# Performance work log

Hardware: AMD Instinct MI355X
Metric: run time of the kernel (lower is better)

The kernel has to match this reference:

```python
import jax, jax.numpy as jnp
import numpy as np

DIM, HK, HV, DK, DV, KC = 2048, 16, 32, 128, 128, 4
B, L = 1, 8192
EPS = 1e-6


def setup_inputs() -> dict:
    key = jax.random.key(0)
    ks = jax.random.split(key, 12)
    conv_dim = 2 * HK * DK + HV * DV  # 8192
    inp = {
        "x": jax.random.normal(ks[0], (B, L, DIM), jnp.float32),
        "cu_seqlens": jnp.array([0, 2048, 4096, 6144, 8192], jnp.int64),
        "Wqkv": jax.random.normal(ks[1], (DIM, conv_dim), jnp.float32) * 0.02,
        "Wz": jax.random.normal(ks[2], (DIM, HV * DV), jnp.float32) * 0.02,
        "Wa": jax.random.normal(ks[3], (DIM, HV), jnp.float32) * 0.02,
        "Wb": jax.random.normal(ks[4], (DIM, HV), jnp.float32) * 0.02,
        "conv_w": jax.random.normal(ks[5], (conv_dim, KC), jnp.float32) * 0.2,
        "A_log": jnp.zeros((HV,), jnp.float32),
        "dt_bias": jnp.ones((HV,), jnp.float32),
        "norm_w": jnp.ones((DV,), jnp.float32),
        "Wout": jax.random.normal(ks[6], (HV * DV, DIM), jnp.float32) * 0.02,
    }
    return inp


def _causal_conv_silu(qkv, conv_w, seq_idx):
    # depthwise causal conv1d with per-sequence masking (channels-last)
    Bb, Ll, C = qkv.shape
    xp = jnp.pad(qkv, ((0, 0), (KC - 1, 0), (0, 0)))
    sp = jnp.pad(seq_idx, ((0, 0), (KC - 1, 0)), constant_values=-1)
    out = jnp.zeros_like(qkv)
    for i in range(KC):
        m = (sp[:, i:i + Ll] == seq_idx)[..., None]
        out = out + conv_w[:, i] * jnp.where(m, xp[:, i:i + Ll], 0.0)
    return jax.nn.silu(out)


def _l2norm(x):
    return x * jax.lax.rsqrt(jnp.sum(x * x, axis=-1, keepdims=True) + EPS)


def reference(x, cu_seqlens, Wqkv, Wz, Wa, Wb, conv_w, A_log, dt_bias, norm_w, Wout):
    Bb, Ll, _ = x.shape
    qkv = x @ Wqkv            # [B,L,conv_dim]
    z = x @ Wz                # [B,L,HV*DV]
    a = x @ Wa                # [B,L,HV]
    b = x @ Wb                # [B,L,HV]

    pos = jnp.arange(Ll)
    seq_idx = jnp.searchsorted(cu_seqlens[1:-1], pos, side="right").astype(jnp.int32)
    seq_idx = jnp.broadcast_to(seq_idx[None, :], (Bb, Ll))

    mixed = _causal_conv_silu(qkv, conv_w, seq_idx)
    key_dim, value_dim = HK * DK, HV * DV
    q, k, v = jnp.split(mixed, [key_dim, 2 * key_dim], axis=-1)
    q = q.reshape(Bb, Ll, HK, DK)
    k = k.reshape(Bb, Ll, HK, DK)
    v = v.reshape(Bb, Ll, HV, DV)
    rep = HV // HK
    q = jnp.repeat(q, rep, axis=2)  # [B,L,HV,DK]
    k = jnp.repeat(k, rep, axis=2)

    # gates
    g = -jnp.exp(A_log) * jax.nn.softplus(a + dt_bias)   # [B,L,HV] (log decay)
    beta = jax.nn.sigmoid(b)                              # [B,L,HV]

    # l2-normed q/k, q scaled
    q = _l2norm(q) * (DK ** -0.5)
    k = _l2norm(k)

    # sequence-start flags for state reset
    starts = jnp.zeros((Ll,), bool).at[cu_seqlens[:-1]].set(True)

    def step(S, inp):
        q_t, k_t, v_t, g_t, b_t, s_t = inp
        S = jnp.where(s_t, 0.0, S)
        S = S * jnp.exp(g_t)[..., None, None]                 # decay
        kv = jnp.einsum("bhk,bhkv->bhv", k_t, S)              # S^T k
        delta = (v_t - kv) * b_t[..., None]
        S = S + k_t[..., :, None] * delta[..., None, :]       # rank-1 delta update
        o = jnp.einsum("bhk,bhkv->bhv", q_t, S)
        return S, o

    S0 = jnp.zeros((Bb, HV, DK, DV), q.dtype)
    xs = (jnp.moveaxis(q, 1, 0), jnp.moveaxis(k, 1, 0), jnp.moveaxis(v, 1, 0),
          jnp.moveaxis(g, 1, 0), jnp.moveaxis(beta, 1, 0), starts)
    _, o = jax.lax.scan(step, S0, xs)                          # [L,B,HV,DV]
    o = jnp.moveaxis(o, 0, 1)                                  # [B,L,HV,DV]

    # gated RMSNorm (gate applied before norm, swish)
    zh = z.reshape(Bb, Ll, HV, DV)
    y = o * jax.nn.silu(zh)
    y = y * jax.lax.rsqrt(jnp.mean(y * y, axis=-1, keepdims=True) + EPS) * norm_w

    return y.reshape(Bb, Ll, HV * DV) @ Wout
```

## Files before the change

kernel.cpp:

```cpp
#include <hip/hip_runtime.h>
#include <hip/hip_bf16.h>
#include <stdint.h>
#include <stdio.h>

#define L_SEQ 8192
#define DIM_ 2048
#define HK_ 16
#define HV_ 32
#define DK_ 128
#define DV_ 128
#define CONV_DIM_ 8192
#define EPS_F 1e-6f

typedef __bf16 bf16;
typedef __bf16 bf16x8 __attribute__((ext_vector_type(8)));
typedef __bf16 bf16x4 __attribute__((ext_vector_type(4)));
typedef __bf16 bf16x2 __attribute__((ext_vector_type(2)));
typedef float f32x4 __attribute__((ext_vector_type(4)));

__device__ __forceinline__ void load_lds16(const void* g, void* l) {
  __builtin_amdgcn_global_load_lds((const __attribute__((address_space(1))) uint32_t*)g,
                                   (__attribute__((address_space(3))) uint32_t*)l,
                                   16, 0, 0);
}

__global__ __launch_bounds__(256) void k_convert(const float4* __restrict__ src,
                                                 bf16x4* __restrict__ dst, int n4) {
  int i = blockIdx.x * 256 + threadIdx.x;
  if (i >= n4) return;
  float4 v = src[i];
  bf16x4 o;
  o[0] = (bf16)v.x; o[1] = (bf16)v.y; o[2] = (bf16)v.z; o[3] = (bf16)v.w;
  dst[i] = o;
}

__global__ __launch_bounds__(256) void k_transpose_cvt(const float* __restrict__ W,
                                                       bf16* __restrict__ Wt, int K, int ldW,
                                                       int n_off) {
  __shared__ float tile[32][33];
  int n0 = blockIdx.x * 32, k0 = blockIdx.y * 32;
  int cx = threadIdx.x & 31, ry = threadIdx.x >> 5;
#pragma unroll
  for (int i = 0; i < 4; i++)
    tile[ry + i * 8][cx] = W[(size_t)(k0 + ry + i * 8) * ldW + n_off + n0 + cx];
  __syncthreads();
#pragma unroll
  for (int i = 0; i < 4; i++) {
    int r = ry + i * 8;
    Wt[(size_t)(n0 + r) * K + k0 + cx] = (bf16)tile[cx][r];
  }
}

template <int BF16_OUT>
__global__ __launch_bounds__(256) void k_gemm_bt(const bf16* __restrict__ A,
                                                 const bf16* __restrict__ Bt,
                                                 void* __restrict__ Cout,
                                                 int M, int N, int K) {
  __shared__ __align__(16) bf16 la[4096];
  __shared__ __align__(16) bf16 lb[4096];
  const int tid = threadIdx.x;
  const int lane = tid & 63;
  const int wave = tid >> 6;
  const int wm = wave >> 1, wn = wave & 1;
  const int bm = blockIdx.y << 7, bn = blockIdx.x << 7;

  f32x4 acc[4][4];
#pragma unroll
  for (int i = 0; i < 4; i++)
#pragma unroll
    for (int j = 0; j < 4; j++) acc[i][j] = (f32x4){0.f, 0.f, 0.f, 0.f};

  const bf16* Ag = A + (size_t)(bm + lane) * K + wave * 8;
  const bf16* Bg = Bt + (size_t)(bn + lane) * K + wave * 8;
  bf16* lA = la + wave * 1024;
  bf16* lB = lb + wave * 1024;
  const size_t rowskip = (size_t)64 * K;

  const int chunk = lane >> 4;
  const int rr = lane & 15;
  const bf16* fa = la + chunk * 1024 + (wm * 64 + rr) * 8;
  const bf16* fb = lb + chunk * 1024 + (wn * 64 + rr) * 8;

  for (int k0 = 0; k0 < K; k0 += 32) {
    __syncthreads();
    load_lds16(Ag + k0, lA);
    load_lds16(Ag + k0 + rowskip, lA + 512);
    load_lds16(Bg + k0, lB);
    load_lds16(Bg + k0 + rowskip, lB + 512);
    __syncthreads();
    bf16x8 af[4], bfr[4];
#pragma unroll
    for (int i = 0; i < 4; i++) {
      af[i] = *(const bf16x8*)(fa + i * 16 * 8);
      bfr[i] = *(const bf16x8*)(fb + i * 16 * 8);
    }
#pragma unroll
    for (int mi = 0; mi < 4; mi++)
#pragma unroll
      for (int ni = 0; ni < 4; ni++)
        acc[mi][ni] = __builtin_amdgcn_mfma_f32_16x16x32_bf16(af[mi], bfr[ni], acc[mi][ni], 0, 0, 0);
  }

  const int col = bn + wn * 64 + rr;
  const int row0 = bm + wm * 64 + (lane >> 4) * 4;
#pragma unroll
  for (int mi = 0; mi < 4; mi++)
#pragma unroll
    for (int ni = 0; ni < 4; ni++)
#pragma unroll
      for (int r = 0; r < 4; r++) {
        int rowi = row0 + mi * 16 + r;
        int coli = col + ni * 16;
        if (BF16_OUT)
          ((bf16*)Cout)[(size_t)rowi * N + coli] = (bf16)acc[mi][ni][r];
        else
          ((float*)Cout)[(size_t)rowi * N + coli] = acc[mi][ni][r];
      }
}

__global__ __launch_bounds__(256) void k_gates(const float* __restrict__ x,
                                               const float* __restrict__ Wa,
                                               const float* __restrict__ Wb,
                                               const float* __restrict__ A_log,
                                               const float* __restrict__ dt_bias,
                                               float* __restrict__ gb) {
  int t = blockIdx.x * 4 + (threadIdx.x >> 6);
  int lane = threadIdx.x & 63;
  int h = lane & 31;
  int isB = lane >> 5;
  const float* W = isB ? Wb : Wa;
  const float* xr = x + (size_t)t * DIM_;
  float a0 = 0.f, a1 = 0.f, a2 = 0.f, a3 = 0.f;
  for (int kk = 0; kk < DIM_; kk += 4) {
    float4 xv = *(const float4*)(xr + kk);
    a0 += xv.x * W[(kk + 0) * 32 + h];
    a1 += xv.y * W[(kk + 1) * 32 + h];
    a2 += xv.z * W[(kk + 2) * 32 + h];
    a3 += xv.w * W[(kk + 3) * 32 + h];
  }
  float acc = (a0 + a1) + (a2 + a3);
  if (isB) {
    gb[(size_t)t * 64 + 32 + h] = 1.f / (1.f + expf(-acc));
  } else {
    float ag = acc + dt_bias[h];
    float sp = (ag > 20.f) ? ag : log1pf(expf(ag));
    gb[(size_t)t * 64 + h] = -expf(A_log[h]) * sp;
  }
}

template <int IS_V>
__global__ __launch_bounds__(128) void k_conv(const bf16* __restrict__ src,
                                              const float* __restrict__ conv_w,
                                              const int* __restrict__ cu, int nseq,
                                              bf16* __restrict__ qn, bf16* __restrict__ kn,
                                              bf16* __restrict__ v) {
  __shared__ float red[2];
  int t = blockIdx.x;
  int grp = blockIdx.y;
  int c = grp * 128 + threadIdx.x;
  int start = 0;
  for (int s = 0; s < nseq; s++) {
    int a = cu[s];
    if (a <= t) start = a;
  }
  float4 w = *(const float4*)(conv_w + (size_t)(c + (IS_V ? 4096 : 0)) * 4);
  float accv = 0.f;
#pragma unroll
  for (int i = 0; i < 4; i++) {
    int tp = t - 3 + i;
    if (tp >= start) {
      float wv = (i == 0) ? w.x : (i == 1) ? w.y : (i == 2) ? w.z : w.w;
      accv += wv * (float)src[(size_t)tp * 4096 + c];
    }
  }
  float val = accv / (1.f + __expf(-accv));
  if (IS_V) {
    v[((size_t)t * HV_ + grp) * DV_ + threadIdx.x] = (bf16)val;
  } else {
    float ss = val * val;
#pragma unroll
    for (int off = 1; off < 64; off <<= 1) ss += __shfl_xor(ss, off);
    if ((threadIdx.x & 63) == 0) red[threadIdx.x >> 6] = ss;
    __syncthreads();
    float tot = red[0] + red[1];
    float scale = rsqrtf(tot + EPS_F);
    if (grp < 16) {
      scale *= 0.08838834764831845f;
      qn[((size_t)t * HK_ + grp) * DK_ + threadIdx.x] = (bf16)(val * scale);
    } else {
      kn[((size_t)t * HK_ + (grp - 16)) * DK_ + threadIdx.x] = (bf16)(val * scale);
    }
  }
}


#define SA_LD 68
#define SUF_LD 65

__device__ __forceinline__ bf16x8 frag256(const bf16* base, int tile, int kk, int lane) {
  int row = tile * 16 + (lane & 15);
  int blk = kk * 4 + (lane >> 4);
  int byte = row * 256 + (((blk & 8) | ((blk & 7) ^ (row & 7))) << 4);
  return *(const bf16x8*)((const char*)base + byte);
}
__device__ __forceinline__ bf16x8 frag128(const bf16* base, int tile, int kk, int lane) {
  int row = tile * 16 + (lane & 15);
  int blk = kk * 4 + (lane >> 4);
  int byte = row * 128 + ((blk ^ (row & 7)) << 4);
  return *(const bf16x8*)((const char*)base + byte);
}
__device__ __forceinline__ bf16x8 ld256v(const bf16* base, int row, int blk) {
  int byte = row * 256 + (((blk & 8) | ((blk & 7) ^ (row & 7))) << 4);
  return *(const bf16x8*)((const char*)base + byte);
}
__device__ __forceinline__ void st128e(bf16* base, int row, int col, float v) {
  int byte = row * 128 + ((((col >> 3) ^ (row & 7)) << 4)) + (col & 7) * 2;
  *(bf16*)((char*)base + byte) = (bf16)v;
}
__device__ __forceinline__ float ld128e(const bf16* base, int row, int col) {
  int byte = row * 128 + ((((col >> 3) ^ (row & 7)) << 4)) + (col & 7) * 2;
  return (float)*(const bf16*)((const char*)base + byte);
}
__device__ __forceinline__ void st256e(bf16* base, int row, int col, float v) {
  int blk = col >> 3;
  int byte = row * 256 + (((blk & 8) | ((blk & 7) ^ (row & 7))) << 4) + (col & 7) * 2;
  *(bf16*)((char*)base + byte) = (bf16)v;
}

__global__ __launch_bounds__(256, 1) void k_scan_chunk(const bf16* __restrict__ qn,
                                                       const bf16* __restrict__ kn,
                                                       const bf16* __restrict__ v,
                                                       const float* __restrict__ gb,
                                                       const int* __restrict__ cu,
                                                       bf16* __restrict__ o) {
  __shared__ __align__(16) bf16 sK[64 * 128];
  __shared__ __align__(16) bf16 sQ[64 * 128];
  __shared__ __align__(16) bf16 sKt[128 * 64];
  __shared__ __align__(16) bf16 sSt[64 * 128];
  __shared__ __align__(16) bf16 sV[64 * 64];
  __shared__ __align__(16) bf16 sM[64 * 64];
  __shared__ __align__(16) bf16 sUt[64 * 64];
  __shared__ float sA[64 * SA_LD];
  __shared__ float sUf[64 * SUF_LD];
  __shared__ float sG2[2][64], sB[2][64], sEg[2][64];

  const int h = blockIdx.y;
  const int hk = h >> 1;
  const int seq = blockIdx.z;
  const int dv0 = blockIdx.x * 64;
  const int tid = threadIdx.x;
  const int lane = tid & 63;
  const int wave = tid >> 6;
  const int w16 = wave * 16;
  const int t0 = cu[seq], t1 = cu[seq + 1];
  if (t0 >= t1) return;

  f32x4 St[2][4];
#pragma unroll
  for (int a = 0; a < 2; a++)
#pragma unroll
    for (int c = 0; c < 4; c++) St[a][c] = (f32x4){0.f, 0.f, 0.f, 0.f};
#pragma unroll
  for (int i = 0; i < 4; i++) ((float4*)sSt)[tid * 4 + i] = (float4){0.f, 0.f, 0.f, 0.f};

  auto stageKQV = [&](int ts) {
#pragma unroll
    for (int it = 0; it < 4; it++) {
      int Bx = (wave * 4 + it) * 64 + lane;
      int r = Bx >> 4, bq = Bx & 15;
      int tr = ts + r; if (tr >= t1) tr = t1 - 1;
      int bs = (bq & 8) | ((bq & 7) ^ (r & 7));
      size_t go = (size_t)tr * (HK_ * DK_) + hk * DK_ + bs * 8;
      load_lds16(kn + go, (char*)sK + (size_t)(wave * 4 + it) * 1024);
      load_lds16(qn + go, (char*)sQ + (size_t)(wave * 4 + it) * 1024);
    }
#pragma unroll
    for (int it = 0; it < 2; it++) {
      int Bx = (wave * 2 + it) * 64 + lane;
      int r = Bx >> 3, bq = Bx & 7;
      int tr = ts + r; if (tr >= t1) tr = t1 - 1;
      int bs = bq ^ (r & 7);
      load_lds16(v + (size_t)tr * (HV_ * DV_) + h * DV_ + dv0 + bs * 8,
                 (char*)sV + (size_t)(wave * 2 + it) * 1024);
    }
  };

  auto prefix = [&](int ts, int pb) {
    int tr = ts + lane;
    float gv = 0.f, bv = 0.f;
    if (tr < t1) {
      gv = gb[(size_t)tr * 64 + h] * 1.44269504088896f;
      bv = gb[(size_t)tr * 64 + 32 + h];
    }
    float ps = gv;
#pragma unroll
    for (int off = 1; off < 64; off <<= 1) {
      float tmp = __shfl_up(ps, off);
      if (lane >= off) ps += tmp;
    }
    sG2[pb][lane] = ps;
    sB[pb][lane] = bv;
    sEg[pb][lane] = exp2f(ps);
  };

  int buf = 0;
  stageKQV(t0);
  if (wave == 0) prefix(t0, 0);
  __syncthreads();

  bool first = true;
  for (int ts = t0; ts < t1; ts += 64) {
    const bool haveNext = (ts + 64 < t1);
    const float* G2 = sG2[buf];
    const float* Bt = sB[buf];
    const float* Eg = sEg[buf];

    f32x4 aKK[4], aQK[4], aKS[4], aQS[4];
#pragma unroll
    for (int c = 0; c < 4; c++) {
      aKK[c] = (f32x4){0.f, 0.f, 0.f, 0.f};
      aQK[c] = (f32x4){0.f, 0.f, 0.f, 0.f};
      aKS[c] = (f32x4){0.f, 0.f, 0.f, 0.f};
      aQS[c] = (f32x4){0.f, 0.f, 0.f, 0.f};
    }
#pragma unroll
    for (int kk = 0; kk < 4; kk++) {
      bf16x8 ak = frag256(sK, wave, kk, lane);
      bf16x8 aq = frag256(sQ, wave, kk, lane);
#pragma unroll
      for (int c = 0; c < 4; c++) {
        if (c <= wave) {
          bf16x8 bk = frag256(sK, c, kk, lane);
          aKK[c] = __builtin_amdgcn_mfma_f32_16x16x32_bf16(ak, bk, aKK[c], 0, 0, 0);
          aQK[c] = __builtin_amdgcn_mfma_f32_16x16x32_bf16(aq, bk, aQK[c], 0, 0, 0);
        }
        if (!first) {
          bf16x8 bs = frag256(sSt, c, kk, lane);
          aKS[c] = __builtin_amdgcn_mfma_f32_16x16x32_bf16(ak, bs, aKS[c], 0, 0, 0);
          aQS[c] = __builtin_amdgcn_mfma_f32_16x16x32_bf16(aq, bs, aQS[c], 0, 0, 0);
        }
      }
    }

    const float G2c = G2[63];
    {
      const int li = lane & 15, lh = lane >> 4;
      float g2s[4];
#pragma unroll
      for (int c = 0; c < 4; c++) g2s[c] = G2[c * 16 + li];
#pragma unroll
      for (int r = 0; r < 4; r++) {
        const int t = w16 + lh * 4 + r;
        const float g2t = G2[t], btv = Bt[t], egt = Eg[t];
#pragma unroll
        for (int c = 0; c < 4; c++) {
          const int s = c * 16 + li;
          const float e = exp2f(g2t - g2s[c]);
          sA[t * SA_LD + s] = (s < t) ? btv * e * aKK[c][r] : 0.f;
          st128e(sM, t, s, (s <= t) ? e * aQK[c][r] : 0.f);
          sUf[t * SUF_LD + s] = btv * (ld128e(sV, t, s) - egt * aKS[c][r]);
        }
      }
    }
    {
      const int t = lane;
      const float sc = exp2f(G2c - G2[t]);
#pragma unroll
      for (int i = 0; i < 4; i++) {
        int dk0 = wave * 32 + i * 8;
        bf16x8 kv = ld256v(sK, t, wave * 4 + i);
#pragma unroll
        for (int j = 0; j < 8; j++) st128e(sKt, dk0 + j, t, (float)kv[j] * sc);
      }
    }
    __syncthreads();

    if (haveNext) {
      stageKQV(ts + 64);
      if (wave == 3) prefix(ts + 64, buf ^ 1);
    }

    for (int b = 0; b < 4; b++) {
      if (wave == 0) {
        const int b16o = b * 16;
        float u[16];
#pragma unroll
        for (int i = 0; i < 16; i++) {
          const int t = b16o + i;
          float x = sUf[t * SUF_LD + lane];
          const float* Ar = &sA[t * SA_LD + b16o];
#pragma unroll
          for (int j = 0; j < i; j++) x -= Ar[j] * u[j];
          u[i] = x;
          sUf[t * SUF_LD + lane] = x;
        }
      }
      __syncthreads();
      if (b < 3) {
        if (wave < 3) {
          const int b16o = b * 16;
          float us[16];
#pragma unroll
          for (int j = 0; j < 16; j++) us[j] = sUf[(b16o + j) * SUF_LD + lane];
          for (int t = b16o + 16 + wave; t < 64; t += 3) {
            float x = sUf[t * SUF_LD + lane];
            const float* Ar = &sA[t * SA_LD + b16o];
#pragma unroll
            for (int j = 0; j < 16; j++) x -= Ar[j] * us[j];
            sUf[t * SUF_LD + lane] = x;
          }
        }
        __syncthreads();
      }
    }

    {
      const int s = lane;
#pragma unroll
      for (int i = 0; i < 16; i++) {
        int dvv = wave * 16 + i;
        st128e(sUt, dvv, s, sUf[s * SUF_LD + dvv]);
      }
    }
    __syncthreads();

    f32x4 aO[4];
#pragma unroll
    for (int c = 0; c < 4; c++)
#pragma unroll
      for (int r = 0; r < 4; r++)
        aO[c][r] = Eg[w16 + (lane >> 4) * 4 + r] * aQS[c][r];
#pragma unroll
    for (int kk = 0; kk < 2; kk++) {
      bf16x8 am = frag128(sM, wave, kk, lane);
#pragma unroll
      for (int c = 0; c < 4; c++) {
        bf16x8 bu = frag128(sUt, c, kk, lane);
        aO[c] = __builtin_amdgcn_mfma_f32_16x16x32_bf16(am, bu, aO[c], 0, 0, 0);
      }
    }
#pragma unroll
    for (int r = 0; r < 4; r++) {
      const int t = w16 + (lane >> 4) * 4 + r;
      if (ts + t < t1) {
#pragma unroll
        for (int c = 0; c < 4; c++)
          o[((size_t)(ts + t) * HV_ + h) * DV_ + dv0 + c * 16 + (lane & 15)] = (bf16)aO[c][r];
      }
    }

    {
      const float egc = Eg[63];
#pragma unroll
      for (int a = 0; a < 2; a++)
#pragma unroll
        for (int c = 0; c < 4; c++)
#pragma unroll
          for (int r = 0; r < 4; r++) St[a][c][r] *= egc;
#pragma unroll
      for (int kk = 0; kk < 2; kk++) {
#pragma unroll
        for (int a = 0; a < 2; a++) {
          bf16x8 akt = frag128(sKt, 2 * wave + a, kk, lane);
#pragma unroll
          for (int c = 0; c < 4; c++) {
            bf16x8 bu = frag128(sUt, c, kk, lane);
            St[a][c] = __builtin_amdgcn_mfma_f32_16x16x32_bf16(akt, bu, St[a][c], 0, 0, 0);
          }
        }
      }
#pragma unroll
      for (int a = 0; a < 2; a++)
#pragma unroll
        for (int c = 0; c < 4; c++)
#pragma unroll
          for (int r = 0; r < 4; r++) {
            int dk = (2 * wave + a) * 16 + (lane >> 4) * 4 + r;
            int dvv = c * 16 + (lane & 15);
            st256e(sSt, dvv, dk, St[a][c][r]);
          }
    }
    first = false;
    buf ^= 1;
    __syncthreads();
  }
}

__global__ __launch_bounds__(256) void k_gatenorm(const bf16* __restrict__ o,
                                                  const bf16* __restrict__ z,
                                                  const float* __restrict__ norm_w,
                                                  bf16* __restrict__ y) {
  int row = blockIdx.x * 4 + (threadIdx.x >> 6);
  int lane = threadIdx.x & 63;
  int i0 = lane * 2;
  bf16x2 ov = *(const bf16x2*)(o + (size_t)row * 128 + i0);
  bf16x2 zv = *(const bf16x2*)(z + (size_t)row * 128 + i0);
  float zf0 = (float)zv[0], zf1 = (float)zv[1];
  float y0 = (float)ov[0] * (zf0 / (1.f + __expf(-zf0)));
  float y1 = (float)ov[1] * (zf1 / (1.f + __expf(-zf1)));
  float ss = y0 * y0 + y1 * y1;
#pragma unroll
  for (int off = 1; off < 64; off <<= 1) ss += __shfl_xor(ss, off);
  float scale = rsqrtf(ss * (1.f / 128.f) + EPS_F);
  float2 nw = *(const float2*)(norm_w + i0);
  bf16x2 out;
  out[0] = (bf16)(y0 * scale * nw.x);
  out[1] = (bf16)(y1 * scale * nw.y);
  *(bf16x2*)(y + (size_t)row * 128 + i0) = out;
}

extern "C" void kernel_launch(void* const* d_in, const int* in_sizes, int n_in,
                              void* d_out, int out_size, void* d_ws, size_t ws_size,
                              hipStream_t stream) {
  const float* x = (const float*)d_in[0];
  const int* cu = (const int*)d_in[1];
  const float* Wqkv = (const float*)d_in[2];
  const float* Wz = (const float*)d_in[3];
  const float* Wa = (const float*)d_in[4];
  const float* Wb = (const float*)d_in[5];
  const float* conv_w = (const float*)d_in[6];
  const float* A_log = (const float*)d_in[7];
  const float* dt_bias = (const float*)d_in[8];
  const float* norm_w = (const float*)d_in[9];
  const float* Wout = (const float*)d_in[10];
  float* out = (float*)d_out;
  const int nseq = in_sizes[1] - 1;

  const size_t MB = 1024 * 1024;
  char* ws = (char*)d_ws;
  bf16* x16   = (bf16*)(ws + 0);
  bf16* WtS   = (bf16*)(ws + 32 * MB);
  bf16* qn    = (bf16*)(ws + 48 * MB);
  bf16* kn    = (bf16*)(ws + 80 * MB);
  bf16* bigA  = (bf16*)(ws + 112 * MB);
  bf16* vbuf  = (bf16*)(ws + 176 * MB);
  float* gb   = (float*)(ws + 240 * MB);
  bf16* z16   = qn;
  bf16* o16   = bigA;
  bf16* y16   = z16;

  if (242 * MB > ws_size) {
    fprintf(stderr, "WORKSPACE TOO SMALL: need %zu, have %zu\n", 242 * MB, ws_size);
    return;
  }

  k_convert<<<(L_SEQ * DIM_ / 4 + 255) / 256, 256, 0, stream>>>((const float4*)x, (bf16x4*)x16,
                                                                L_SEQ * DIM_ / 4);
  k_gates<<<L_SEQ / 4, 256, 0, stream>>>(x, Wa, Wb, A_log, dt_bias, gb);

  k_transpose_cvt<<<dim3(4096 / 32, DIM_ / 32), 256, 0, stream>>>(Wqkv, WtS, DIM_, CONV_DIM_, 0);
  k_gemm_bt<1><<<dim3(4096 / 128, L_SEQ / 128), 256, 0, stream>>>(x16, WtS, bigA, L_SEQ, 4096, DIM_);
  k_conv<0><<<dim3(L_SEQ, 32), 128, 0, stream>>>(bigA, conv_w, cu, nseq, qn, kn, vbuf);

  k_transpose_cvt<<<dim3(4096 / 32, DIM_ / 32), 256, 0, stream>>>(Wqkv, WtS, DIM_, CONV_DIM_, 4096);
  k_gemm_bt<1><<<dim3(4096 / 128, L_SEQ / 128), 256, 0, stream>>>(x16, WtS, bigA, L_SEQ, 4096, DIM_);
  k_conv<1><<<dim3(L_SEQ, 32), 128, 0, stream>>>(bigA, conv_w, cu, nseq, qn, kn, vbuf);

  k_scan_chunk<<<dim3(2, HV_, nseq), 256, 0, stream>>>(qn, kn, vbuf, gb, cu, o16);

  k_transpose_cvt<<<dim3(4096 / 32, DIM_ / 32), 256, 0, stream>>>(Wz, WtS, DIM_, 4096, 0);
  k_gemm_bt<1><<<dim3(4096 / 128, L_SEQ / 128), 256, 0, stream>>>(x16, WtS, z16, L_SEQ, 4096, DIM_);

  k_gatenorm<<<L_SEQ * HV_ / 4, 256, 0, stream>>>(o16, z16, norm_w, y16);

  k_transpose_cvt<<<dim3(DIM_ / 32, 4096 / 32), 256, 0, stream>>>(Wout, WtS, 4096, DIM_, 0);
  k_gemm_bt<0><<<dim3(DIM_ / 128, L_SEQ / 128), 256, 0, stream>>>(y16, WtS, out, L_SEQ, DIM_, 4096);
}
```

Measured before the change: 2.303 ms.

## Double scan block to 512 threads with split Q/K wave roles; batch elementwise kernels

The chunked delta-rule scan kernel now runs 8 waves instead of 4. Waves are split into two groups: one handles the Q-side products and output, the other the K-side products, the triangular solve and the state update. Each wave now holds only a quarter-size state tile. This raises parallelism in the latency-bound scan (only 256 blocks) at the cost of more barrier participants. The convert, conv and gatenorm kernels also process several rows or elements per thread, which cuts block count and launch overhead.

Result: faster. 2.139 ms (-7.1%).

```diff
diff --git a/kernel.cpp b/kernel.cpp
--- a/kernel.cpp
+++ b/kernel.cpp
@@ -26,12 +26,15 @@
 
 __global__ __launch_bounds__(256) void k_convert(const float4* __restrict__ src,
                                                  bf16x4* __restrict__ dst, int n4) {
-  int i = blockIdx.x * 256 + threadIdx.x;
-  if (i >= n4) return;
-  float4 v = src[i];
-  bf16x4 o;
-  o[0] = (bf16)v.x; o[1] = (bf16)v.y; o[2] = (bf16)v.z; o[3] = (bf16)v.w;
-  dst[i] = o;
+#pragma unroll
+  for (int it = 0; it < 8; it++) {
+    int i = blockIdx.x * 2048 + it * 256 + threadIdx.x;
+    if (i >= n4) continue;
+    float4 v = src[i];
+    bf16x4 o;
+    o[0] = (bf16)v.x; o[1] = (bf16)v.y; o[2] = (bf16)v.z; o[3] = (bf16)v.w;
+    dst[i] = o;
+  }
 }
 
 __global__ __launch_bounds__(256) void k_transpose_cvt(const float* __restrict__ W,
@@ -155,40 +158,43 @@
                                               bf16* __restrict__ qn, bf16* __restrict__ kn,
                                               bf16* __restrict__ v) {
   __shared__ float red[2];
-  int t = blockIdx.x;
-  int grp = blockIdx.y;
-  int c = grp * 128 + threadIdx.x;
-  int start = 0;
-  for (int s = 0; s < nseq; s++) {
-    int a = cu[s];
-    if (a <= t) start = a;
-  }
+  const int grp = blockIdx.y;
+  const int c = grp * 128 + threadIdx.x;
   float4 w = *(const float4*)(conv_w + (size_t)(c + (IS_V ? 4096 : 0)) * 4);
-  float accv = 0.f;
-#pragma unroll
-  for (int i = 0; i < 4; i++) {
-    int tp = t - 3 + i;
-    if (tp >= start) {
-      float wv = (i == 0) ? w.x : (i == 1) ? w.y : (i == 2) ? w.z : w.w;
-      accv += wv * (float)src[(size_t)tp * 4096 + c];
-    }
-  }
-  float val = accv / (1.f + __expf(-accv));
-  if (IS_V) {
-    v[((size_t)t * HV_ + grp) * DV_ + threadIdx.x] = (bf16)val;
-  } else {
-    float ss = val * val;
-#pragma unroll
-    for (int off = 1; off < 64; off <<= 1) ss += __shfl_xor(ss, off);
-    if ((threadIdx.x & 63) == 0) red[threadIdx.x >> 6] = ss;
-    __syncthreads();
-    float tot = red[0] + red[1];
-    float scale = rsqrtf(tot + EPS_F);
-    if (grp < 16) {
-      scale *= 0.08838834764831845f;
-      qn[((size_t)t * HK_ + grp) * DK_ + threadIdx.x] = (bf16)(val * scale);
+  for (int it = 0; it < 8; it++) {
+    int t = blockIdx.x * 8 + it;
+    int start = 0;
+    for (int s = 0; s < nseq; s++) {
+      int a = cu[s];
+      if (a <= t) start = a;
+    }
+    float accv = 0.f;
+#pragma unroll
+    for (int i = 0; i < 4; i++) {
+      int tp = t - 3 + i;
+      if (tp >= start) {
+        float wv = (i == 0) ? w.x : (i == 1) ? w.y : (i == 2) ? w.z : w.w;
+        accv += wv * (float)src[(size_t)tp * 4096 + c];
+      }
+    }
+    float val = accv / (1.f + __expf(-accv));
+    if (IS_V) {
+      v[((size_t)t * HV_ + grp) * DV_ + threadIdx.x] = (bf16)val;
     } else {
-      kn[((size_t)t * HK_ + (grp - 16)) * DK_ + threadIdx.x] = (bf16)(val * scale);
+      float ss = val * val;
+#pragma unroll
+      for (int off = 1; off < 64; off <<= 1) ss += __shfl_xor(ss, off);
+      if ((threadIdx.x & 63) == 0) red[threadIdx.x >> 6] = ss;
+      __syncthreads();
+      float tot = red[0] + red[1];
+      float scale = rsqrtf(tot + EPS_F);
+      if (grp < 16) {
+        scale *= 0.08838834764831845f;
+        qn[((size_t)t * HK_ + grp) * DK_ + threadIdx.x] = (bf16)(val * scale);
+      } else {
+        kn[((size_t)t * HK_ + (grp - 16)) * DK_ + threadIdx.x] = (bf16)(val * scale);
+      }
+      __syncthreads();
     }
   }
 }
@@ -227,7 +233,7 @@
   *(bf16*)((char*)base + byte) = (bf16)v;
 }
 
-__global__ __launch_bounds__(256, 1) void k_scan_chunk(const bf16* __restrict__ qn,
+__global__ __launch_bounds__(512, 2) void k_scan_chunk(const bf16* __restrict__ qn,
                                                        const bf16* __restrict__ kn,
                                                        const bf16* __restrict__ v,
                                                        const float* __restrict__ gb,
@@ -251,37 +257,35 @@
   const int tid = threadIdx.x;
   const int lane = tid & 63;
   const int wave = tid >> 6;
-  const int w16 = wave * 16;
+  const int w4 = wave & 3;
+  const int grp = wave >> 2;
   const int t0 = cu[seq], t1 = cu[seq + 1];
   if (t0 >= t1) return;
 
-  f32x4 St[2][4];
-#pragma unroll
-  for (int a = 0; a < 2; a++)
-#pragma unroll
-    for (int c = 0; c < 4; c++) St[a][c] = (f32x4){0.f, 0.f, 0.f, 0.f};
-#pragma unroll
-  for (int i = 0; i < 4; i++) ((float4*)sSt)[tid * 4 + i] = (float4){0.f, 0.f, 0.f, 0.f};
+  f32x4 St[4];
+#pragma unroll
+  for (int c = 0; c < 4; c++) St[c] = (f32x4){0.f, 0.f, 0.f, 0.f};
+  ((float4*)sSt)[tid] = (float4){0.f, 0.f, 0.f, 0.f};
+  ((float4*)sSt)[tid + 512] = (float4){0.f, 0.f, 0.f, 0.f};
 
   auto stageKQV = [&](int ts) {
 #pragma unroll
-    for (int it = 0; it < 4; it++) {
-      int Bx = (wave * 4 + it) * 64 + lane;
+    for (int it = 0; it < 2; it++) {
+      int Bx = (wave * 2 + it) * 64 + lane;
       int r = Bx >> 4, bq = Bx & 15;
       int tr = ts + r; if (tr >= t1) tr = t1 - 1;
       int bs = (bq & 8) | ((bq & 7) ^ (r & 7));
       size_t go = (size_t)tr * (HK_ * DK_) + hk * DK_ + bs * 8;
-      load_lds16(kn + go, (char*)sK + (size_t)(wave * 4 + it) * 1024);
-      load_lds16(qn + go, (char*)sQ + (size_t)(wave * 4 + it) * 1024);
-    }
-#pragma unroll
-    for (int it = 0; it < 2; it++) {
-      int Bx = (wave * 2 + it) * 64 + lane;
+      load_lds16(kn + go, (char*)sK + (size_t)(wave * 2 + it) * 1024);
+      load_lds16(qn + go, (char*)sQ + (size_t)(wave * 2 + it) * 1024);
+    }
+    {
+      int Bx = wave * 64 + lane;
       int r = Bx >> 3, bq = Bx & 7;
       int tr = ts + r; if (tr >= t1) tr = t1 - 1;
       int bs = bq ^ (r & 7);
       load_lds16(v + (size_t)tr * (HV_ * DV_) + h * DV_ + dv0 + bs * 8,
-                 (char*)sV + (size_t)(wave * 2 + it) * 1024);
+                 (char*)sV + (size_t)wave * 1024);
     }
   };
 
@@ -315,69 +319,76 @@
     const float* Bt = sB[buf];
     const float* Eg = sEg[buf];
 
-    f32x4 aKK[4], aQK[4], aKS[4], aQS[4];
+    f32x4 accA[4], accB[4];
 #pragma unroll
     for (int c = 0; c < 4; c++) {
-      aKK[c] = (f32x4){0.f, 0.f, 0.f, 0.f};
-      aQK[c] = (f32x4){0.f, 0.f, 0.f, 0.f};
-      aKS[c] = (f32x4){0.f, 0.f, 0.f, 0.f};
-      aQS[c] = (f32x4){0.f, 0.f, 0.f, 0.f};
-    }
+      accA[c] = (f32x4){0.f, 0.f, 0.f, 0.f};
+      accB[c] = (f32x4){0.f, 0.f, 0.f, 0.f};
+    }
+    const bf16* opA = grp ? sK : sQ;
 #pragma unroll
     for (int kk = 0; kk < 4; kk++) {
-      bf16x8 ak = frag256(sK, wave, kk, lane);
-      bf16x8 aq = frag256(sQ, wave, kk, lane);
+      bf16x8 af = frag256(opA, w4, kk, lane);
 #pragma unroll
       for (int c = 0; c < 4; c++) {
-        if (c <= wave) {
+        if (c <= w4) {
           bf16x8 bk = frag256(sK, c, kk, lane);
-          aKK[c] = __builtin_amdgcn_mfma_f32_16x16x32_bf16(ak, bk, aKK[c], 0, 0, 0);
-          aQK[c] = __builtin_amdgcn_mfma_f32_16x16x32_bf16(aq, bk, aQK[c], 0, 0, 0);
+          accA[c] = __builtin_amdgcn_mfma_f32_16x16x32_bf16(af, bk, accA[c], 0, 0, 0);
         }
         if (!first) {
-          bf16x8 bs = frag256(sSt, c, kk, lane);
-          aKS[c] = __builtin_amdgcn_mfma_f32_16x16x32_bf16(ak, bs, aKS[c], 0, 0, 0);
-          aQS[c] = __builtin_amdgcn_mfma_f32_16x16x32_bf16(aq, bs, aQS[c], 0, 0, 0);
+          bf16x8 bs_ = frag256(sSt, c, kk, lane);
+          accB[c] = __builtin_amdgcn_mfma_f32_16x16x32_bf16(af, bs_, accB[c], 0, 0, 0);
         }
       }
     }
 
     const float G2c = G2[63];
+    const int li = lane & 15, lh = lane >> 4;
     {
-      const int li = lane & 15, lh = lane >> 4;
       float g2s[4];
 #pragma unroll
       for (int c = 0; c < 4; c++) g2s[c] = G2[c * 16 + li];
-#pragma unroll
-      for (int r = 0; r < 4; r++) {
-        const int t = w16 + lh * 4 + r;
-        const float g2t = G2[t], btv = Bt[t], egt = Eg[t];
-#pragma unroll
-        for (int c = 0; c < 4; c++) {
-          const int s = c * 16 + li;
-          const float e = exp2f(g2t - g2s[c]);
-          sA[t * SA_LD + s] = (s < t) ? btv * e * aKK[c][r] : 0.f;
-          st128e(sM, t, s, (s <= t) ? e * aQK[c][r] : 0.f);
-          sUf[t * SUF_LD + s] = btv * (ld128e(sV, t, s) - egt * aKS[c][r]);
-        }
-      }
-    }
-    {
-      const int t = lane;
-      const float sc = exp2f(G2c - G2[t]);
-#pragma unroll
-      for (int i = 0; i < 4; i++) {
-        int dk0 = wave * 32 + i * 8;
-        bf16x8 kv = ld256v(sK, t, wave * 4 + i);
-#pragma unroll
-        for (int j = 0; j < 8; j++) st128e(sKt, dk0 + j, t, (float)kv[j] * sc);
+      if (grp) {
+#pragma unroll
+        for (int r = 0; r < 4; r++) {
+          const int t = w4 * 16 + lh * 4 + r;
+          const float g2t = G2[t], btv = Bt[t], egt = Eg[t];
+#pragma unroll
+          for (int c = 0; c < 4; c++) {
+            const int s = c * 16 + li;
+            const float e = exp2f(g2t - g2s[c]);
+            sA[t * SA_LD + s] = (s < t) ? btv * e * accA[c][r] : 0.f;
+            sUf[t * SUF_LD + s] = btv * (ld128e(sV, t, s) - egt * accB[c][r]);
+          }
+        }
+      } else {
+#pragma unroll
+        for (int r = 0; r < 4; r++) {
+          const int t = w4 * 16 + lh * 4 + r;
+          const float g2t = G2[t];
+#pragma unroll
+          for (int c = 0; c < 4; c++) {
+            const int s = c * 16 + li;
+            const float e = exp2f(g2t - g2s[c]);
+            st128e(sM, t, s, (s <= t) ? e * accA[c][r] : 0.f);
+          }
+        }
+        const int tt = lane;
+        const float sc = exp2f(G2c - G2[tt]);
+#pragma unroll
+        for (int i = 0; i < 4; i++) {
+          int dk0 = w4 * 32 + i * 8;
+          bf16x8 kv = ld256v(sK, tt, w4 * 4 + i);
+#pragma unroll
+          for (int j = 0; j < 8; j++) st128e(sKt, dk0 + j, tt, (float)kv[j] * sc);
+        }
       }
     }
     __syncthreads();
 
     if (haveNext) {
       stageKQV(ts + 64);
-      if (wave == 3) prefix(ts + 64, buf ^ 1);
+      if (wave == 7) prefix(ts + 64, buf ^ 1);
     }
 
     for (int b = 0; b < 4; b++) {
@@ -397,12 +408,12 @@
       }
       __syncthreads();
       if (b < 3) {
-        if (wave < 3) {
+        if (wave >= 1 && wave <= 6) {
           const int b16o = b * 16;
           float us[16];
 #pragma unroll
           for (int j = 0; j < 16; j++) us[j] = sUf[(b16o + j) * SUF_LD + lane];
-          for (int t = b16o + 16 + wave; t < 64; t += 3) {
+          for (int t = b16o + 16 + (wave - 1); t < 64; t += 6) {
             float x = sUf[t * SUF_LD + lane];
             const float* Ar = &sA[t * SA_LD + b16o];
 #pragma unroll
@@ -417,68 +428,63 @@
     {
       const int s = lane;
 #pragma unroll
-      for (int i = 0; i < 16; i++) {
-        int dvv = wave * 16 + i;
+      for (int i = 0; i < 8; i++) {
+        int dvv = wave * 8 + i;
         st128e(sUt, dvv, s, sUf[s * SUF_LD + dvv]);
       }
     }
     __syncthreads();
 
-    f32x4 aO[4];
-#pragma unroll
-    for (int c = 0; c < 4; c++)
-#pragma unroll
-      for (int r = 0; r < 4; r++)
-        aO[c][r] = Eg[w16 + (lane >> 4) * 4 + r] * aQS[c][r];
-#pragma unroll
-    for (int kk = 0; kk < 2; kk++) {
-      bf16x8 am = frag128(sM, wave, kk, lane);
-#pragma unroll
-      for (int c = 0; c < 4; c++) {
-        bf16x8 bu = frag128(sUt, c, kk, lane);
-        aO[c] = __builtin_amdgcn_mfma_f32_16x16x32_bf16(am, bu, aO[c], 0, 0, 0);
-      }
-    }
-#pragma unroll
-    for (int r = 0; r < 4; r++) {
-      const int t = w16 + (lane >> 4) * 4 + r;
-      if (ts + t < t1) {
-#pragma unroll
-        for (int c = 0; c < 4; c++)
-          o[((size_t)(ts + t) * HV_ + h) * DV_ + dv0 + c * 16 + (lane & 15)] = (bf16)aO[c][r];
+    if (!grp) {
+      f32x4 aO[4];
+#pragma unroll
+      for (int c = 0; c < 4; c++)
+#pragma unroll
+        for (int r = 0; r < 4; r++)
+          aO[c][r] = Eg[w4 * 16 + lh * 4 + r] * accB[c][r];
+#pragma unroll
+      for (int kk = 0; kk < 2; kk++) {
+        bf16x8 am = frag128(sM, w4, kk, lane);
+#pragma unroll
+        for (int c = 0; c < 4; c++) {
+          bf16x8 bu = frag128(sUt, c, kk, lane);
+          aO[c] = __builtin_amdgcn_mfma_f32_16x16x32_bf16(am, bu, aO[c], 0, 0, 0);
+        }
+      }
+#pragma unroll
+      for (int r = 0; r < 4; r++) {
+        const int t = w4 * 16 + lh * 4 + r;
+        if (ts + t < t1) {
+#pragma unroll
+          for (int c = 0; c < 4; c++)
+            o[((size_t)(ts + t) * HV_ + h) * DV_ + dv0 + c * 16 + li] = (bf16)aO[c][r];
+        }
       }
     }
 
     {
       const float egc = Eg[63];
 #pragma unroll
-      for (int a = 0; a < 2; a++)
-#pragma unroll
-        for (int c = 0; c < 4; c++)
-#pragma unroll
-          for (int r = 0; r < 4; r++) St[a][c][r] *= egc;
+      for (int c = 0; c < 4; c++)
+#pragma unroll
+        for (int r = 0; r < 4; r++) St[c][r] *= egc;
 #pragma unroll
       for (int kk = 0; kk < 2; kk++) {
-#pragma unroll
-        for (int a = 0; a < 2; a++) {
-          bf16x8 akt = frag128(sKt, 2 * wave + a, kk, lane);
-#pragma unroll
-          for (int c = 0; c < 4; c++) {
-            bf16x8 bu = frag128(sUt, c, kk, lane);
-            St[a][c] = __builtin_amdgcn_mfma_f32_16x16x32_bf16(akt, bu, St[a][c], 0, 0, 0);
-          }
-        }
-      }
-#pragma unroll
-      for (int a = 0; a < 2; a++)
-#pragma unroll
-        for (int c = 0; c < 4; c++)
-#pragma unroll
-          for (int r = 0; r < 4; r++) {
-            int dk = (2 * wave + a) * 16 + (lane >> 4) * 4 + r;
-            int dvv = c * 16 + (lane & 15);
-            st256e(sSt, dvv, dk, St[a][c][r]);
-          }
+        bf16x8 akt = frag128(sKt, wave, kk, lane);
+#pragma unroll
+        for (int c = 0; c < 4; c++) {
+          bf16x8 bu = frag128(sUt, c, kk, lane);
+          St[c] = __builtin_amdgcn_mfma_f32_16x16x32_bf16(akt, bu, St[c], 0, 0, 0);
+        }
+      }
+#pragma unroll
+      for (int c = 0; c < 4; c++)
+#pragma unroll
+        for (int r = 0; r < 4; r++) {
+          int dk = wave * 16 + lh * 4 + r;
+          int dvv = c * 16 + li;
+          st256e(sSt, dvv, dk, St[c][r]);
+        }
     }
     first = false;
     buf ^= 1;
@@ -490,23 +496,26 @@
                                                   const bf16* __restrict__ z,
                                                   const float* __restrict__ norm_w,
                                                   bf16* __restrict__ y) {
-  int row = blockIdx.x * 4 + (threadIdx.x >> 6);
   int lane = threadIdx.x & 63;
   int i0 = lane * 2;
-  bf16x2 ov = *(const bf16x2*)(o + (size_t)row * 128 + i0);
-  bf16x2 zv = *(const bf16x2*)(z + (size_t)row * 128 + i0);
-  float zf0 = (float)zv[0], zf1 = (float)zv[1];
-  float y0 = (float)ov[0] * (zf0 / (1.f + __expf(-zf0)));
-  float y1 = (float)ov[1] * (zf1 / (1.f + __expf(-zf1)));
-  float ss = y0 * y0 + y1 * y1;
-#pragma unroll
-  for (int off = 1; off < 64; off <<= 1) ss += __shfl_xor(ss, off);
-  float scale = rsqrtf(ss * (1.f / 128.f) + EPS_F);
   float2 nw = *(const float2*)(norm_w + i0);
-  bf16x2 out;
-  out[0] = (bf16)(y0 * scale * nw.x);
-  out[1] = (bf16)(y1 * scale * nw.y);
-  *(bf16x2*)(y + (size_t)row * 128 + i0) = out;
+#pragma unroll
+  for (int it = 0; it < 16; it++) {
+    int row = blockIdx.x * 64 + it * 4 + (threadIdx.x >> 6);
+    bf16x2 ov = *(const bf16x2*)(o + (size_t)row * 128 + i0);
+    bf16x2 zv = *(const bf16x2*)(z + (size_t)row * 128 + i0);
+    float zf0 = (float)zv[0], zf1 = (float)zv[1];
+    float y0 = (float)ov[0] * (zf0 / (1.f + __expf(-zf0)));
+    float y1 = (float)ov[1] * (zf1 / (1.f + __expf(-zf1)));
+    float ss = y0 * y0 + y1 * y1;
+#pragma unroll
+    for (int off = 1; off < 64; off <<= 1) ss += __shfl_xor(ss, off);
+    float scale = rsqrtf(ss * (1.f / 128.f) + EPS_F);
+    bf16x2 out;
+    out[0] = (bf16)(y0 * scale * nw.x);
+    out[1] = (bf16)(y1 * scale * nw.y);
+    *(bf16x2*)(y + (size_t)row * 128 + i0) = out;
+  }
 }
 
 extern "C" void kernel_launch(void* const* d_in, const int* in_sizes, int n_in,
@@ -544,24 +553,24 @@
     return;
   }
 
-  k_convert<<<(L_SEQ * DIM_ / 4 + 255) / 256, 256, 0, stream>>>((const float4*)x, (bf16x4*)x16,
-                                                                L_SEQ * DIM_ / 4);
+  k_convert<<<L_SEQ * DIM_ / 4 / 2048, 256, 0, stream>>>((const float4*)x, (bf16x4*)x16,
+                                                         L_SEQ * DIM_ / 4);
   k_gates<<<L_SEQ / 4, 256, 0, stream>>>(x, Wa, Wb, A_log, dt_bias, gb);
 
   k_transpose_cvt<<<dim3(4096 / 32, DIM_ / 32), 256, 0, stream>>>(Wqkv, WtS, DIM_, CONV_DIM_, 0);
   k_gemm_bt<1><<<dim3(4096 / 128, L_SEQ / 128), 256, 0, stream>>>(x16, WtS, bigA, L_SEQ, 4096, DIM_);
-  k_conv<0><<<dim3(L_SEQ, 32), 128, 0, stream>>>(bigA, conv_w, cu, nseq, qn, kn, vbuf);
+  k_conv<0><<<dim3(L_SEQ / 8, 32), 128, 0, stream>>>(bigA, conv_w, cu, nseq, qn, kn, vbuf);
 
   k_transpose_cvt<<<dim3(4096 / 32, DIM_ / 32), 256, 0, stream>>>(Wqkv, WtS, DIM_, CONV_DIM_, 4096);
   k_gemm_bt<1><<<dim3(4096 / 128, L_SEQ / 128), 256, 0, stream>>>(x16, WtS, bigA, L_SEQ, 4096, DIM_);
-  k_conv<1><<<dim3(L_SEQ, 32), 128, 0, stream>>>(bigA, conv_w, cu, nseq, qn, kn, vbuf);
-
-  k_scan_chunk<<<dim3(2, HV_, nseq), 256, 0, stream>>>(qn, kn, vbuf, gb, cu, o16);
+  k_conv<1><<<dim3(L_SEQ / 8, 32), 128, 0, stream>>>(bigA, conv_w, cu, nseq, qn, kn, vbuf);
+
+  k_scan_chunk<<<dim3(2, HV_, nseq), 512, 0, stream>>>(qn, kn, vbuf, gb, cu, o16);
 
   k_transpose_cvt<<<dim3(4096 / 32, DIM_ / 32), 256, 0, stream>>>(Wz, WtS, DIM_, 4096, 0);
   k_gemm_bt<1><<<dim3(4096 / 128, L_SEQ / 128), 256, 0, stream>>>(x16, WtS, z16, L_SEQ, 4096, DIM_);
 
-  k_gatenorm<<<L_SEQ * HV_ / 4, 256, 0, stream>>>(o16, z16, norm_w, y16);
+  k_gatenorm<<<L_SEQ * HV_ / 64, 256, 0, stream>>>(o16, z16, norm_w, y16);
 
   k_transpose_cvt<<<dim3(DIM_ / 32, 4096 / 32), 256, 0, stream>>>(Wout, WtS, 4096, DIM_, 0);
   k_gemm_bt<0><<<dim3(DIM_ / 128, L_SEQ / 128), 256, 0, stream>>>(y16, WtS, out, L_SEQ, DIM_, 4096);
```
